# Kernel tuning notes

Hardware: AMD Instinct MI355X
Metric: run time of the kernel (lower is better)

## Reference

```python
import jax, jax.numpy as jnp
import numpy as np
from jax import lax

B, L, DDYN, DSTAT, H = 512, 64, 16, 8, 512
N_BANK, C_CAND, K_TOP, N_PROTO = 50000, 1024, 16, 8
T_TARG, Q_QUANT = 2, 3
TEMP = 0.2


def _l2norm(x, eps=1e-12):
    # matches torch.nn.functional.normalize: x / max(||x||, eps)
    n = jnp.sqrt(jnp.sum(x * x, axis=-1, keepdims=True))
    return x / jnp.maximum(n, eps)


def setup_inputs() -> dict:
    key = jax.random.key(0)
    ks = jax.random.split(key, 24)
    s = 0.02
    inp = {
        'sequence_values': jax.random.normal(ks[0], (B, L, DDYN), jnp.float32),
        'sequence_masks': jnp.ones((B, L), jnp.float32),
        'static_values': jax.random.normal(ks[1], (B, DSTAT), jnp.float32),
        'bank_keys': jax.random.normal(ks[2], (N_BANK, H), jnp.float32),
        'bank_values': jax.random.normal(ks[3], (N_BANK, H), jnp.float32),
        'candidate_indices': jax.random.randint(ks[4], (B, C_CAND), 0, N_BANK, jnp.int64),
        # encoder params (SequenceEncoder stand-in: masked-mean + linear + relu)
        'W_seq': jax.random.normal(ks[5], (DDYN, H), jnp.float32) * s,
        'W_stat': jax.random.normal(ks[6], (DSTAT, H), jnp.float32) * s,
        'b_enc': jnp.zeros((H,), jnp.float32),
        # retrieval / prototype / fusion params
        'W_q': jax.random.normal(ks[7], (H, H), jnp.float32) * s,
        'b_q': jnp.zeros((H,), jnp.float32),
        'prototype_tokens': jax.random.normal(ks[8], (N_PROTO, H), jnp.float32) * 0.02,
        'W_tr': jax.random.normal(ks[9], (2 * H, H), jnp.float32) * s,
        'b_tr': jnp.zeros((H,), jnp.float32),
        'W_gate': jax.random.normal(ks[10], (3 * H, H), jnp.float32) * s,
        'b_gate': jnp.zeros((H,), jnp.float32),
        'W_out': jax.random.normal(ks[11], (H, H), jnp.float32) * s,
        'b_out': jnp.zeros((H,), jnp.float32),
        # per-target heads stacked: [T, H, Q] and [T, H]
        'W_quant': jax.random.normal(ks[12], (T_TARG, H, Q_QUANT), jnp.float32) * s,
        'b_quant': jnp.zeros((T_TARG, Q_QUANT), jnp.float32),
        'W_ev': jax.random.normal(ks[13], (T_TARG, H), jnp.float32) * s,
        'b_ev': jnp.zeros((T_TARG,), jnp.float32),
    }
    return inp


def reference(sequence_values, sequence_masks, static_values, bank_keys, bank_values,
              candidate_indices, W_seq, W_stat, b_enc, W_q, b_q, prototype_tokens,
              W_tr, b_tr, W_gate, b_gate, W_out, b_out, W_quant, b_quant, W_ev, b_ev):
    # --- encoder (masked mean pool + linear + relu stand-in for SequenceEncoder) ---
    m = sequence_masks[..., None]                                   # [B,L,1]
    pooled = (sequence_values * m).sum(1) / jnp.maximum(m.sum(1), 1e-6)
    local_hidden = jax.nn.relu(pooled @ W_seq + static_values @ W_stat + b_enc)  # [B,H]

    # --- normalized query ---
    query = _l2norm(local_hidden @ W_q + b_q)                       # [B,H]

    # --- donor retrieval: gather + dot + topk + softmax + weighted sum ---
    cand_keys = bank_keys[candidate_indices]                        # [B,C,H]
    sim = jnp.einsum('bch,bh->bc', cand_keys, query)                # [B,C]
    top_scores, top_pos = lax.top_k(sim, K_TOP)                     # [B,K]
    weights = jax.nn.softmax(top_scores / max(TEMP, 1e-6), axis=-1)
    sel_idx = jnp.take_along_axis(candidate_indices, top_pos, axis=1)  # [B,K]
    donor_hidden = jnp.einsum('bk,bkh->bh', weights, bank_values[sel_idx])

    # --- prototype attention ---
    protos_n = _l2norm(prototype_tokens)                            # [P,H]
    pw = jax.nn.softmax(query @ protos_n.T, axis=-1)                # [B,P]
    proto_hidden = pw @ prototype_tokens                            # [B,H]

    # --- transfer / gate / fuse (dropout is identity at eval) ---
    transfer = jax.nn.relu(jnp.concatenate([donor_hidden, proto_hidden], -1) @ W_tr + b_tr)
    gate = jax.nn.sigmoid(
        jnp.concatenate([local_hidden, donor_hidden, proto_hidden], -1) @ W_gate + b_gate)
    fused = gate * local_hidden + (1.0 - gate) * transfer
    fused = jax.nn.relu(fused @ W_out + b_out)                      # [B,H]

    # --- heads: sorted quantiles [B,T,Q] and event logits [B,T] ---
    quant = jnp.sort(jnp.einsum('bh,thq->btq', fused, W_quant) + b_quant, axis=-1)
    logit = jnp.einsum('bh,th->bt', fused, W_ev) + b_ev
    return jnp.concatenate([quant.reshape(quant.shape[0], -1), logit], axis=-1)  # [B, T*Q+T]
```

## Files before the change

kernel.cpp:

```cpp
#include <hip/hip_runtime.h>
#include <hip/hip_bf16.h>

typedef __hip_bfloat16 bf16;

__device__ __forceinline__ float lo16(unsigned u){ return __uint_as_float(u << 16); }
__device__ __forceinline__ float hi16(unsigned u){ return __uint_as_float(u & 0xffff0000u); }

#define Bn 512
#define Hn 512
#define Cn 1024
#define Kn 16
#define NBANK 50000
#define NIDPAD 50176

__device__ __forceinline__ int clamp_id(int id){
    return (id < 0) ? 0 : ((id >= NBANK) ? (NBANK - 1) : id);
}

#define QRAW_OFF 0
#define F1_OFF   0
#define G_OFF    262144
#define DONOR_OFF (G_OFF + 262144)
#define PROTO_OFF (G_OFF + 524288)
#define SIM_OFF  1048576
#define F2_OFF   1048576
#define GATE_OFF 1572864
#define TR_OFF   1835008
#define WS_FLOATS 2097152

#define HIST_I   0
#define CURSOR_I NIDPAD
#define OFFS_I   (2*NIDPAD)
#define CHPREF_I (2*NIDPAD + NIDPAD)

__global__ __launch_bounds__(256) void k_enc(
    const float* __restrict__ seq, const float* __restrict__ mask, const float* __restrict__ stat,
    const float* __restrict__ W_seq, const float* __restrict__ W_stat, const float* __restrict__ b_enc,
    const int* __restrict__ cand32, float* __restrict__ ws)
{
    const int b = blockIdx.x, t = threadIdx.x;
    const int h0 = 2*t, h1 = 2*t + 1;

    {
        const int c64 = ((cand32[1] | cand32[3] | cand32[5] | cand32[7]) == 0) ? 1 : 0;
        int* hist = (int*)(ws + GATE_OFF) + HIST_I;
        #pragma unroll
        for (int u = 0; u < 4; u++) {
            int idx = b*Cn + u*256 + t;
            atomicAdd(&hist[clamp_id(cand32[(size_t)idx << c64])], 1);
        }
    }

    __shared__ float s_pool[16], s_stat[8];
    if (t < 16) {
        float acc = 0.f, ms = 0.f;
        for (int l = 0; l < 64; l++) {
            float m = mask[b*64 + l];
            ms  += m;
            acc += seq[(b*64 + l)*16 + t] * m;
        }
        s_pool[t] = acc / fmaxf(ms, 1e-6f);
    } else if (t < 24) {
        s_stat[t - 16] = stat[b*8 + (t - 16)];
    }
    __syncthreads();
    float a0 = b_enc[h0], a1 = b_enc[h1];
    #pragma unroll
    for (int j = 0; j < 16; j++) {
        float2 wv = *(const float2*)(W_seq + j*Hn + h0);
        a0 += s_pool[j]*wv.x; a1 += s_pool[j]*wv.y;
    }
    #pragma unroll
    for (int j = 0; j < 8; j++) {
        float2 wv = *(const float2*)(W_stat + j*Hn + h0);
        a0 += s_stat[j]*wv.x; a1 += s_stat[j]*wv.y;
    }
    float* g = ws + G_OFF + (size_t)b*Hn;
    g[h0] = fmaxf(a0, 0.f); g[h1] = fmaxf(a1, 0.f);
}

__global__ __launch_bounds__(256) void k_qgemm_sk(
    const float* __restrict__ W, const float* __restrict__ bias,
    const float* __restrict__ in, int in_stride, int in_off,
    float* __restrict__ outp)
{
    const int ct = blockIdx.x, rt = blockIdx.y, kz = blockIdx.z, t = threadIdx.x;
    __shared__ float lt[64][132];
    {
        int r = t >> 2, c0 = (t & 3)*32;
        const float* src = in + (size_t)(rt*64 + r)*in_stride + in_off + kz*128 + c0;
        #pragma unroll
        for (int i = 0; i < 8; i++)
            *(float4*)&lt[r][c0 + i*4] = *(const float4*)(src + i*4);
    }
    __syncthreads();
    const int col0 = ct*64 + (t & 15)*4, rbase = (t >> 4)*4;
    float acc[4][4];
    if (kz == 0) {
        float4 bv = *(const float4*)(bias + col0);
        #pragma unroll
        for (int i = 0; i < 4; i++) { acc[i][0]=bv.x; acc[i][1]=bv.y; acc[i][2]=bv.z; acc[i][3]=bv.w; }
    } else {
        #pragma unroll
        for (int i = 0; i < 4; i++) { acc[i][0]=0; acc[i][1]=0; acc[i][2]=0; acc[i][3]=0; }
    }
    const float* wp = W + (size_t)(kz*128)*Hn + col0;
    #pragma unroll 4
    for (int k = 0; k < 128; k++) {
        float4 wv = *(const float4*)(wp + (size_t)k*Hn);
        #pragma unroll
        for (int i = 0; i < 4; i++) {
            float a = lt[rbase + i][k];
            acc[i][0] += a*wv.x; acc[i][1] += a*wv.y; acc[i][2] += a*wv.z; acc[i][3] += a*wv.w;
        }
    }
    #pragma unroll
    for (int i = 0; i < 4; i++) {
        float* op = outp + (size_t)(rt*64 + rbase + i)*Hn + col0;
        atomicAdd(op+0, acc[i][0]); atomicAdd(op+1, acc[i][1]);
        atomicAdd(op+2, acc[i][2]); atomicAdd(op+3, acc[i][3]);
    }
}

__global__ __launch_bounds__(64) void k_qnorm(float* __restrict__ ws)
{
    const int b = blockIdx.x, lane = threadIdx.x;
    float* qr = ws + QRAW_OFF + (size_t)b*Hn + lane*8;
    float4 qa = *(const float4*)qr, qb = *(const float4*)(qr + 4);
    float ss = qa.x*qa.x + qa.y*qa.y + qa.z*qa.z + qa.w*qa.w
             + qb.x*qb.x + qb.y*qb.y + qb.z*qb.z + qb.w*qb.w;
    #pragma unroll
    for (int o = 32; o; o >>= 1) ss += __shfl_xor(ss, o);
    float inv = 1.f / fmaxf(sqrtf(ss), 1e-12f);
    qa.x *= inv; qa.y *= inv; qa.z *= inv; qa.w *= inv;
    qb.x *= inv; qb.y *= inv; qb.z *= inv; qb.w *= inv;
    *(float4*)qr = qa; *(float4*)(qr + 4) = qb;
}

__global__ __launch_bounds__(256) void k_scanA(
    const int* __restrict__ hist, int* __restrict__ offs, int* __restrict__ chsum)
{
    __shared__ int s[256];
    const int t = threadIdx.x, g = blockIdx.x*256 + t;
    const int v = hist[g];
    s[t] = v; __syncthreads();
    #pragma unroll
    for (int off = 1; off < 256; off <<= 1) {
        int x = (t >= off) ? s[t - off] : 0;
        __syncthreads();
        s[t] += x;
        __syncthreads();
    }
    offs[g] = s[t] - v;
    if (t == 255) chsum[blockIdx.x] = s[255];
}

__global__ __launch_bounds__(256) void k_scanB(int* __restrict__ chsum)
{
    __shared__ int s[256];
    const int t = threadIdx.x;
    const int v = (t < 196) ? chsum[t] : 0;
    s[t] = v; __syncthreads();
    #pragma unroll
    for (int off = 1; off < 256; off <<= 1) {
        int x = (t >= off) ? s[t - off] : 0;
        __syncthreads();
        s[t] += x;
        __syncthreads();
    }
    if (t < 196) chsum[t] = s[t] - v;
}

__global__ __launch_bounds__(256) void k_scatter(
    const int* __restrict__ cand32, int* __restrict__ cursor,
    const int* __restrict__ offs, const int* __restrict__ chpref,
    unsigned* __restrict__ refs)
{
    const int i = blockIdx.x*256 + threadIdx.x;
    const int c64 = ((cand32[1] | cand32[3] | cand32[5] | cand32[7]) == 0) ? 1 : 0;
    const int id = clamp_id(cand32[(size_t)i << c64]);
    const int pos = atomicAdd(&cursor[id], 1);
    refs[offs[id] + chpref[id >> 8] + pos] = (unsigned)i;
}

__global__ __launch_bounds__(256) void k_dotinv(
    const float* __restrict__ bank_keys, const unsigned* __restrict__ refs,
    const int* __restrict__ offs, const int* __restrict__ chpref,
    float* __restrict__ ws)
{
    const int id = blockIdx.x*4 + (threadIdx.x >> 6);
    const int lane = threadIdx.x & 63;
    const int start = offs[id]     + chpref[id >> 8];
    const int end   = offs[id + 1] + chpref[(id + 1) >> 8];
    if (start >= end) return;

    const float* kp = bank_keys + (size_t)id*Hn + lane*8;
    float4 ka = *(const float4*)kp, kb = *(const float4*)(kp + 4);
    const float* qbase = ws + QRAW_OFF;
    float* simw = ws + SIM_OFF;

    for (int r = start; r < end; r += 4) {
        const int nn = end - r;
        unsigned rv0 = refs[r];
        unsigned rv1 = refs[nn > 1 ? r + 1 : r];
        unsigned rv2 = refs[nn > 2 ? r + 2 : r];
        unsigned rv3 = refs[nn > 3 ? r + 3 : r];
        const float* q0 = qbase + (size_t)(rv0 >> 10)*Hn + lane*8;
        const float* q1 = qbase + (size_t)(rv1 >> 10)*Hn + lane*8;
        const float* q2 = qbase + (size_t)(rv2 >> 10)*Hn + lane*8;
        const float* q3 = qbase + (size_t)(rv3 >> 10)*Hn + lane*8;
        float4 a0 = *(const float4*)q0, b0 = *(const float4*)(q0 + 4);
        float4 a1 = *(const float4*)q1, b1 = *(const float4*)(q1 + 4);
        float4 a2 = *(const float4*)q2, b2 = *(const float4*)(q2 + 4);
        float4 a3 = *(const float4*)q3, b3 = *(const float4*)(q3 + 4);
        float s0 = ka.x*a0.x + ka.y*a0.y + ka.z*a0.z + ka.w*a0.w
                 + kb.x*b0.x + kb.y*b0.y + kb.z*b0.z + kb.w*b0.w;
        float s1 = ka.x*a1.x + ka.y*a1.y + ka.z*a1.z + ka.w*a1.w
                 + kb.x*b1.x + kb.y*b1.y + kb.z*b1.z + kb.w*b1.w;
        float s2 = ka.x*a2.x + ka.y*a2.y + ka.z*a2.z + ka.w*a2.w
                 + kb.x*b2.x + kb.y*b2.y + kb.z*b2.z + kb.w*b2.w;
        float s3 = ka.x*a3.x + ka.y*a3.y + ka.z*a3.z + ka.w*a3.w
                 + kb.x*b3.x + kb.y*b3.y + kb.z*b3.z + kb.w*b3.w;
        #pragma unroll
        for (int o = 32; o; o >>= 1) {
            s0 += __shfl_xor(s0, o); s1 += __shfl_xor(s1, o);
            s2 += __shfl_xor(s2, o); s3 += __shfl_xor(s3, o);
        }
        if (lane == 0) {
            simw[rv0] = s0;
            if (nn > 1) simw[rv1] = s1;
            if (nn > 2) simw[rv2] = s2;
            if (nn > 3) simw[rv3] = s3;
        }
    }
}

__global__ __launch_bounds__(256) void k_select(
    const float* __restrict__ bank_values, const int* __restrict__ cand32,
    const float* __restrict__ proto, float* __restrict__ ws)
{
    const int b = blockIdx.x, t = threadIdx.x;
    const int w = t >> 6, lane = t & 63;
    const int h0 = 2*t, h1 = 2*t + 1;
    const int c64 = ((cand32[1] | cand32[3] | cand32[5] | cand32[7]) == 0) ? 1 : 0;

    __shared__ __align__(16) float s_sim[Cn];
    __shared__ float s_bv[4]; __shared__ int s_bi[4];
    __shared__ float s_topv[Kn]; __shared__ int s_sel[Kn];
    __shared__ float s_w[Kn];
    __shared__ float s_score[8], s_pw[8];

    *(float4*)&s_sim[t*4] = *(const float4*)(ws + SIM_OFF + (size_t)b*Cn + t*4);

    const float* qr = ws + QRAW_OFF + (size_t)b*Hn + lane*8;
    float4 qa = *(const float4*)qr, qb = *(const float4*)(qr + 4);
    float qv[8] = {qa.x, qa.y, qa.z, qa.w, qb.x, qb.y, qb.z, qb.w};
    __syncthreads();

    for (int k = 0; k < Kn; k++) {
        float best = -1e30f; int bi = 0x7fffffff;
        for (int i = t; i < Cn; i += 256) {
            float v = s_sim[i];
            if (v > best || (v == best && i < bi)) { best = v; bi = i; }
        }
        #pragma unroll
        for (int o = 32; o; o >>= 1) {
            float ov = __shfl_xor(best, o); int oi = __shfl_xor(bi, o);
            if (ov > best || (ov == best && oi < bi)) { best = ov; bi = oi; }
        }
        if (lane == 0) { s_bv[w] = best; s_bi[w] = bi; }
        __syncthreads();
        if (t == 0) {
            float bv = s_bv[0]; int bbi = s_bi[0];
            for (int x = 1; x < 4; x++)
                if (s_bv[x] > bv || (s_bv[x] == bv && s_bi[x] < bbi)) { bv = s_bv[x]; bbi = s_bi[x]; }
            if (bbi < 0 || bbi >= Cn) bbi = 0;
            s_topv[k] = bv; s_sel[k] = bbi; s_sim[bbi] = -1e30f;
        }
        __syncthreads();
    }

    if (t == 0) {
        float m = s_topv[0];
        float e[Kn], ssum = 0.f;
        for (int k = 0; k < Kn; k++) { e[k] = __expf((s_topv[k] - m) * 5.0f); ssum += e[k]; }
        float inv = 1.f / ssum;
        for (int k = 0; k < Kn; k++) s_w[k] = e[k] * inv;
    }
    for (int p = w; p < 8; p += 4) {
        const float* pp = proto + (size_t)p*Hn + lane*8;
        float4 pa = *(const float4*)pp, pb = *(const float4*)(pp + 4);
        float f[8] = {pa.x, pa.y, pa.z, pa.w, pb.x, pb.y, pb.z, pb.w};
        float dq = 0.f, sq = 0.f;
        #pragma unroll
        for (int i = 0; i < 8; i++) { dq += f[i]*qv[i]; sq += f[i]*f[i]; }
        #pragma unroll
        for (int o = 32; o; o >>= 1) { dq += __shfl_xor(dq, o); sq += __shfl_xor(sq, o); }
        if (lane == 0) s_score[p] = dq / fmaxf(sqrtf(sq), 1e-12f);
    }
    __syncthreads();
    if (t == 0) {
        float m = s_score[0];
        for (int p = 1; p < 8; p++) m = fmaxf(m, s_score[p]);
        float e[8], ssum = 0.f;
        for (int p = 0; p < 8; p++) { e[p] = __expf(s_score[p] - m); ssum += e[p]; }
        float inv = 1.f / ssum;
        for (int p = 0; p < 8; p++) s_pw[p] = e[p] * inv;
    }
    __syncthreads();

    {
        float a0 = 0.f, a1 = 0.f;
        #pragma unroll
        for (int k = 0; k < Kn; k++) {
            int id = clamp_id(cand32[(size_t)(b*Cn + s_sel[k]) << c64]);
            float2 v = *(const float2*)(bank_values + (size_t)id*Hn + h0);
            a0 += s_w[k]*v.x; a1 += s_w[k]*v.y;
        }
        float* gd = ws + DONOR_OFF + (size_t)b*Hn;
        gd[h0] = a0; gd[h1] = a1;
    }
    {
        float a0 = 0.f, a1 = 0.f;
        #pragma unroll
        for (int p = 0; p < 8; p++) {
            float2 v = *(const float2*)(proto + (size_t)p*Hn + h0);
            a0 += s_pw[p]*v.x; a1 += s_pw[p]*v.y;
        }
        float* gp = ws + PROTO_OFF + (size_t)b*Hn;
        gp[h0] = a0; gp[h1] = a1;
    }
}

__global__ __launch_bounds__(256) void k_gatetr_sk(
    const float* __restrict__ W_tr, const float* __restrict__ b_tr,
    const float* __restrict__ W_gate, const float* __restrict__ b_gate,
    float* __restrict__ ws)
{
    const int ct = blockIdx.x, rt = blockIdx.y, z = blockIdx.z, t = threadIdx.x;
    const int isGate = (z < 6);
    const int slice = isGate ? z : (z - 6);
    const float* W  = isGate ? W_gate : W_tr;
    const int gcol = isGate ? slice*256 : 512 + slice*256;
    const float* srcbase = ws + G_OFF + (size_t)(gcol >> 9)*262144 + (gcol & 511);
    float* outp = ws + (isGate ? GATE_OFF : TR_OFF);

    __shared__ float lt[32][260];
    {
        int r = t >> 3, c0 = (t & 7)*32;
        const float* src = srcbase + (size_t)(rt*32 + r)*Hn + c0;
        #pragma unroll
        for (int i = 0; i < 8; i++)
            *(float4*)&lt[r][c0 + i*4] = *(const float4*)(src + i*4);
    }
    __syncthreads();
    const int col0 = ct*128 + (t & 31)*4, rbase = (t >> 5)*4;
    float acc[4][4];
    if (slice == 0) {
        const float* bias = isGate ? b_gate : b_tr;
        float4 bv = *(const float4*)(bias + col0);
        #pragma unroll
        for (int i = 0; i < 4; i++) { acc[i][0]=bv.x; acc[i][1]=bv.y; acc[i][2]=bv.z; acc[i][3]=bv.w; }
    } else {
        #pragma unroll
        for (int i = 0; i < 4; i++) { acc[i][0]=0; acc[i][1]=0; acc[i][2]=0; acc[i][3]=0; }
    }
    const float* wp = W + (size_t)(slice*256)*Hn + col0;
    #pragma unroll 4
    for (int k = 0; k < 256; k++) {
        float4 wv = *(const float4*)(wp + (size_t)k*Hn);
        #pragma unroll
        for (int i = 0; i < 4; i++) {
            float a = lt[rbase + i][k];
            acc[i][0] += a*wv.x; acc[i][1] += a*wv.y; acc[i][2] += a*wv.z; acc[i][3] += a*wv.w;
        }
    }
    #pragma unroll
    for (int i = 0; i < 4; i++) {
        float* op = outp + (size_t)(rt*32 + rbase + i)*Hn + col0;
        atomicAdd(op+0, acc[i][0]); atomicAdd(op+1, acc[i][1]);
        atomicAdd(op+2, acc[i][2]); atomicAdd(op+3, acc[i][3]);
    }
}

__global__ __launch_bounds__(256) void k_f1ew(float* __restrict__ ws)
{
    const int i4 = blockIdx.x*256 + threadIdx.x;
    const int row = i4 >> 7, c = (i4 & 127)*4;
    float4 lc = *(const float4*)(ws + G_OFF + (size_t)row*Hn + c);
    float4 ga = *(const float4*)(ws + GATE_OFF + (size_t)row*Hn + c);
    float4 tr = *(const float4*)(ws + TR_OFF + (size_t)row*Hn + c);
    float4 r;
    float s;
    s = 1.f/(1.f + __expf(-ga.x)); r.x = s*lc.x + (1.f-s)*fmaxf(tr.x, 0.f);
    s = 1.f/(1.f + __expf(-ga.y)); r.y = s*lc.y + (1.f-s)*fmaxf(tr.y, 0.f);
    s = 1.f/(1.f + __expf(-ga.z)); r.z = s*lc.z + (1.f-s)*fmaxf(tr.z, 0.f);
    s = 1.f/(1.f + __expf(-ga.w)); r.w = s*lc.w + (1.f-s)*fmaxf(tr.w, 0.f);
    *(float4*)(ws + F1_OFF + (size_t)row*Hn + c) = r;
}

__global__ __launch_bounds__(64) void k_heads(
    const float* __restrict__ W_quant, const float* __restrict__ b_quant,
    const float* __restrict__ W_ev, const float* __restrict__ b_ev,
    const float* __restrict__ ws_ro, float* __restrict__ out)
{
    const int b = blockIdx.x, lane = threadIdx.x;
    const float* fr = ws_ro + F2_OFF + (size_t)b*Hn + lane*8;
    float4 fa = *(const float4*)fr, fb = *(const float4*)(fr + 4);
    float fv[8] = {fmaxf(fa.x,0.f), fmaxf(fa.y,0.f), fmaxf(fa.z,0.f), fmaxf(fa.w,0.f),
                   fmaxf(fb.x,0.f), fmaxf(fb.y,0.f), fmaxf(fb.z,0.f), fmaxf(fb.w,0.f)};
    float acc[8];
    #pragma unroll
    for (int o = 0; o < 8; o++) acc[o] = 0.f;
    #pragma unroll
    for (int i = 0; i < 8; i++) {
        int h = lane*8 + i;
        float fh = fv[i];
        acc[0] += fh*W_quant[(0*Hn + h)*3 + 0];
        acc[1] += fh*W_quant[(0*Hn + h)*3 + 1];
        acc[2] += fh*W_quant[(0*Hn + h)*3 + 2];
        acc[3] += fh*W_quant[(1*Hn + h)*3 + 0];
        acc[4] += fh*W_quant[(1*Hn + h)*3 + 1];
        acc[5] += fh*W_quant[(1*Hn + h)*3 + 2];
        acc[6] += fh*W_ev[0*Hn + h];
        acc[7] += fh*W_ev[1*Hn + h];
    }
    #pragma unroll
    for (int o = 0; o < 8; o++) {
        #pragma unroll
        for (int s = 32; s; s >>= 1) acc[o] += __shfl_xor(acc[o], s);
    }
    if (lane == 0) {
        float q[6];
        for (int o = 0; o < 6; o++) q[o] = acc[o] + b_quant[o];
        #pragma unroll
        for (int tt = 0; tt < 2; tt++) {
            float a = q[tt*3], bb = q[tt*3+1], c = q[tt*3+2];
            float mn = fminf(a, fminf(bb, c)), mx = fmaxf(a, fmaxf(bb, c));
            float md = a + bb + c - mn - mx;
            q[tt*3] = mn; q[tt*3+1] = md; q[tt*3+2] = mx;
        }
        for (int o = 0; o < 6; o++) out[b*8 + o] = q[o];
        out[b*8 + 6] = acc[6] + b_ev[0];
        out[b*8 + 7] = acc[7] + b_ev[1];
    }
}

__device__ __forceinline__ float lds_f(const void* p, int i, int f32){
    return f32 ? ((const float*)p)[i] : __bfloat162float(((const bf16*)p)[i]);
}
__device__ __forceinline__ float2 ldpair(const void* p, int elt, int f32){
    if (f32) return ((const float2*)p)[elt >> 1];
    unsigned u = ((const unsigned*)p)[elt >> 1];
    return make_float2(lo16(u), hi16(u));
}
__device__ __forceinline__ void ld8(const void* p, int elt, int f32, float* v){
    if (f32){
        const float4* q = (const float4*)((const float*)p + elt);
        float4 a = q[0], b = q[1];
        v[0]=a.x; v[1]=a.y; v[2]=a.z; v[3]=a.w; v[4]=b.x; v[5]=b.y; v[6]=b.z; v[7]=b.w;
    } else {
        uint4 u = *(const uint4*)((const bf16*)p + elt);
        v[0]=lo16(u.x); v[1]=hi16(u.x); v[2]=lo16(u.y); v[3]=hi16(u.y);
        v[4]=lo16(u.z); v[5]=hi16(u.z); v[6]=lo16(u.w); v[7]=hi16(u.w);
    }
}
__device__ __forceinline__ void st_out(void* o, int i, int f32, float v){
    if (f32) ((float*)o)[i] = v; else ((bf16*)o)[i] = __float2bfloat16(v);
}

__global__ __launch_bounds__(256) void k_fused(
    const void* __restrict__ seq, const void* __restrict__ mask, const void* __restrict__ stat,
    const void* __restrict__ bank_keys, const void* __restrict__ bank_values,
    const int* __restrict__ cand32,
    const void* __restrict__ W_seq, const void* __restrict__ W_stat, const void* __restrict__ b_enc,
    const void* __restrict__ W_q, const void* __restrict__ b_q,
    const void* __restrict__ proto,
    const void* __restrict__ W_tr, const void* __restrict__ b_tr,
    const void* __restrict__ W_gate, const void* __restrict__ b_gate,
    const void* __restrict__ W_out, const void* __restrict__ b_out,
    const void* __restrict__ W_quant, const void* __restrict__ b_quant,
    const void* __restrict__ W_ev, const void* __restrict__ b_ev,
    void* __restrict__ out)
{
    const int b = blockIdx.x, t = threadIdx.x;
    const int w = t >> 6, lane = t & 63;
    const int h0 = 2*t, h1 = 2*t + 1;
    const int f32 = (((const unsigned short*)mask)[0] == 0) ? 1 : 0;
    const int c64 = ((cand32[1] | cand32[3] | cand32[5] | cand32[7]) == 0) ? 1 : 0;

    __shared__ __align__(16) float s_pool[16];
    __shared__ __align__(16) float s_stat[8];
    __shared__ __align__(16) float g[1536];
    __shared__ __align__(16) float s_q[Hn];
    __shared__ __align__(16) float s_sim[Cn];
    __shared__ __align__(16) float f1[Hn];
    __shared__ __align__(16) float f2[Hn];
    __shared__ float s_part[4], s_ss;
    __shared__ float s_bv[4]; __shared__ int s_bi[4];
    __shared__ float s_topv[Kn]; __shared__ int s_sel[Kn];
    __shared__ float s_w[Kn];
    __shared__ float s_score[8], s_pw[8];
    __shared__ float s_head[8][4];

    if (t < 16) {
        float acc = 0.f, ms = 0.f;
        for (int l = 0; l < 64; l++) {
            float m = lds_f(mask, b*64 + l, f32);
            ms  += m;
            acc += lds_f(seq, (b*64 + l)*16 + t, f32) * m;
        }
        s_pool[t] = acc / fmaxf(ms, 1e-6f);
    } else if (t < 24) {
        s_stat[t - 16] = lds_f(stat, b*8 + (t - 16), f32);
    }
    __syncthreads();
    {
        float a0 = lds_f(b_enc, h0, f32), a1 = lds_f(b_enc, h1, f32);
        #pragma unroll
        for (int j = 0; j < 16; j++) {
            float2 wv = ldpair(W_seq, j*Hn + h0, f32);
            a0 += s_pool[j]*wv.x; a1 += s_pool[j]*wv.y;
        }
        #pragma unroll
        for (int j = 0; j < 8; j++) {
// ... 131 lines not shown
        gt0 += gj*wv.x; gt1 += gj*wv.y;
    }
    gt0 = 1.f/(1.f + __expf(-gt0)); gt1 = 1.f/(1.f + __expf(-gt1));
    f1[h0] = gt0*g[h0] + (1.f - gt0)*tr0;
    f1[h1] = gt1*g[h1] + (1.f - gt1)*tr1;
    __syncthreads();
    {
        float o0 = lds_f(b_out, h0, f32), o1 = lds_f(b_out, h1, f32);
        #pragma unroll 4
        for (int j = 0; j < Hn; j++) {
            float fj = f1[j];
            float2 wv = ldpair(W_out, j*Hn + h0, f32);
            o0 += fj*wv.x; o1 += fj*wv.y;
        }
        o0 = fmaxf(o0, 0.f); o1 = fmaxf(o1, 0.f);
        f2[h0] = o0; f2[h1] = o1;
    }
    __syncthreads();
    {
        float acc[8];
        #pragma unroll
        for (int o = 0; o < 8; o++) acc[o] = 0.f;
        for (int h = t; h < Hn; h += 256) {
            float fh = f2[h];
            acc[0] += fh*lds_f(W_quant, (0*Hn + h)*3 + 0, f32);
            acc[1] += fh*lds_f(W_quant, (0*Hn + h)*3 + 1, f32);
            acc[2] += fh*lds_f(W_quant, (0*Hn + h)*3 + 2, f32);
            acc[3] += fh*lds_f(W_quant, (1*Hn + h)*3 + 0, f32);
            acc[4] += fh*lds_f(W_quant, (1*Hn + h)*3 + 1, f32);
            acc[5] += fh*lds_f(W_quant, (1*Hn + h)*3 + 2, f32);
            acc[6] += fh*lds_f(W_ev, 0*Hn + h, f32);
            acc[7] += fh*lds_f(W_ev, 1*Hn + h, f32);
        }
        #pragma unroll
        for (int o = 0; o < 8; o++) {
            float v = acc[o];
            #pragma unroll
            for (int s = 32; s; s >>= 1) v += __shfl_xor(v, s);
            if (lane == 0) s_head[o][w] = v;
        }
        __syncthreads();
        if (t == 0) {
            float q[6];
            for (int o = 0; o < 6; o++)
                q[o] = s_head[o][0] + s_head[o][1] + s_head[o][2] + s_head[o][3] + lds_f(b_quant, o, f32);
            #pragma unroll
            for (int tt = 0; tt < 2; tt++) {
                float a = q[tt*3], bb = q[tt*3+1], c = q[tt*3+2];
                float mn = fminf(a, fminf(bb, c)), mx = fmaxf(a, fmaxf(bb, c));
                float md = a + bb + c - mn - mx;
                q[tt*3] = mn; q[tt*3+1] = md; q[tt*3+2] = mx;
            }
            for (int o = 0; o < 6; o++) st_out(out, b*8 + o, f32, q[o]);
            float l0 = s_head[6][0] + s_head[6][1] + s_head[6][2] + s_head[6][3] + lds_f(b_ev, 0, f32);
            float l1 = s_head[7][0] + s_head[7][1] + s_head[7][2] + s_head[7][3] + lds_f(b_ev, 1, f32);
            st_out(out, b*8 + 6, f32, l0);
            st_out(out, b*8 + 7, f32, l1);
        }
    }
}

extern "C" void kernel_launch(void* const* d_in, const int* in_sizes, int n_in,
                              void* d_out, int out_size, void* d_ws, size_t ws_size,
                              hipStream_t stream) {
    static const int expect[22] = {
        512*64*16, 512*64, 512*8, 50000*512, 50000*512, 512*1024,
        16*512, 8*512, 512, 512*512, 512, 8*512,
        1024*512, 512, 1536*512, 512, 512*512, 512,
        2*512*3, 2*3, 2*512, 2
    };
    if (n_in != 22 || out_size != 512*8) return;
    for (int i = 0; i < 22; i++) if (in_sizes[i] != expect[i]) return;

    if (ws_size < (size_t)WS_FLOATS * 4) {
        k_fused<<<Bn, 256, 0, stream>>>(
            d_in[0], d_in[1], d_in[2], d_in[3], d_in[4], (const int*)d_in[5],
            d_in[6], d_in[7], d_in[8], d_in[9], d_in[10], d_in[11],
            d_in[12], d_in[13], d_in[14], d_in[15], d_in[16], d_in[17],
            d_in[18], d_in[19], d_in[20], d_in[21], d_out);
        return;
    }

    float* ws = (float*)d_ws;
    int* iws = (int*)(ws + GATE_OFF);
    int* hist   = iws + HIST_I;
    int* cursor = iws + CURSOR_I;
    int* offs   = iws + OFFS_I;
    int* chpref = iws + CHPREF_I;
    unsigned* refs = (unsigned*)(ws + DONOR_OFF);

    hipMemsetAsync(ws + QRAW_OFF, 0, (size_t)512*512*4, stream);
    hipMemsetAsync(hist, 0, (size_t)2*NIDPAD*4, stream);
    hipMemsetAsync(ws + TR_OFF, 0, (size_t)512*512*4, stream);

    k_enc<<<Bn, 256, 0, stream>>>((const float*)d_in[0], (const float*)d_in[1],
                                  (const float*)d_in[2], (const float*)d_in[6],
                                  (const float*)d_in[7], (const float*)d_in[8],
                                  (const int*)d_in[5], ws);
    k_scanA<<<NIDPAD/256, 256, 0, stream>>>(hist, offs, chpref);
    k_scanB<<<1, 256, 0, stream>>>(chpref);
    k_scatter<<<(Bn*Cn)/256, 256, 0, stream>>>((const int*)d_in[5], cursor, offs, chpref, refs);
    k_qgemm_sk<<<dim3(8, 8, 4), 256, 0, stream>>>(
        (const float*)d_in[9], (const float*)d_in[10], ws + G_OFF, 512, 0, ws + QRAW_OFF);
    k_qnorm<<<Bn, 64, 0, stream>>>(ws);
    k_dotinv<<<NBANK/4, 256, 0, stream>>>((const float*)d_in[3], refs, offs, chpref, ws);
    k_select<<<Bn, 256, 0, stream>>>((const float*)d_in[4], (const int*)d_in[5],
                                     (const float*)d_in[11], ws);
    hipMemsetAsync(ws + GATE_OFF, 0, (size_t)512*512*4, stream);
    hipMemsetAsync(ws + F2_OFF, 0, (size_t)512*512*4, stream);
    k_gatetr_sk<<<dim3(4, 16, 10), 256, 0, stream>>>(
        (const float*)d_in[12], (const float*)d_in[13],
        (const float*)d_in[14], (const float*)d_in[15], ws);
    k_f1ew<<<256, 256, 0, stream>>>(ws);
    k_qgemm_sk<<<dim3(8, 8, 4), 256, 0, stream>>>(
        (const float*)d_in[16], (const float*)d_in[17], ws + F1_OFF, 512, 0, ws + F2_OFF);
    k_heads<<<Bn, 64, 0, stream>>>((const float*)d_in[18], (const float*)d_in[19],
                                   (const float*)d_in[20], (const float*)d_in[21],
                                   ws, (float*)d_out);
}
```

Measured before the change: 546.8 us.

## Replace split-K atomics with partial buffers, single-pass scan, pipelined dot kernel

The split-K GEMMs now write plain float4 partial results into separate workspace slabs, and the consumers (qnorm, f1ew, heads) sum those partials. This removes the float atomics and most of the large memsets. The two-level scan is merged into one kernel that takes block bases from a global atomic counter. The dot-inverse kernel is software-pipelined with double-buffered loads, shuffles refs from a register, and reduces four dot products at once. The trade-off is extra reads of the partial buffers and a workspace layout that has to stay consistent across every stage.

```diff
diff --git a/kernel.cpp b/kernel.cpp
--- a/kernel.cpp
+++ b/kernel.cpp
@@ -17,21 +17,21 @@
     return (id < 0) ? 0 : ((id >= NBANK) ? (NBANK - 1) : id);
 }
 
-#define QRAW_OFF 0
-#define F1_OFF   0
-#define G_OFF    262144
-#define DONOR_OFF (G_OFF + 262144)
-#define PROTO_OFF (G_OFF + 524288)
+#define A_OFF    0
+#define B_OFF    262144
+#define C_OFF    524288
+#define D_OFF    786432
 #define SIM_OFF  1048576
-#define F2_OFF   1048576
-#define GATE_OFF 1572864
-#define TR_OFF   1835008
+#define ELO_OFF  1048576
+#define EHI_OFF  1310720
+#define F_OFF    1572864
+#define G_OFF2   1835008
 #define WS_FLOATS 2097152
 
 #define HIST_I   0
 #define CURSOR_I NIDPAD
-#define OFFS_I   (2*NIDPAD)
-#define CHPREF_I (2*NIDPAD + NIDPAD)
+#define GTOT_I   (2*NIDPAD)
+#define OFFS_I   (2*NIDPAD + 256)
 
 __global__ __launch_bounds__(256) void k_enc(
     const float* __restrict__ seq, const float* __restrict__ mask, const float* __restrict__ stat,
@@ -43,7 +43,7 @@
 
     {
         const int c64 = ((cand32[1] | cand32[3] | cand32[5] | cand32[7]) == 0) ? 1 : 0;
-        int* hist = (int*)(ws + GATE_OFF) + HIST_I;
+        int* hist = (int*)(ws + F_OFF) + HIST_I;
         #pragma unroll
         for (int u = 0; u < 4; u++) {
             int idx = b*Cn + u*256 + t;
@@ -75,20 +75,51 @@
         float2 wv = *(const float2*)(W_stat + j*Hn + h0);
         a0 += s_stat[j]*wv.x; a1 += s_stat[j]*wv.y;
     }
-    float* g = ws + G_OFF + (size_t)b*Hn;
+    float* g = ws + B_OFF + (size_t)b*Hn;
     g[h0] = fmaxf(a0, 0.f); g[h1] = fmaxf(a1, 0.f);
 }
 
-__global__ __launch_bounds__(256) void k_qgemm_sk(
+__global__ __launch_bounds__(256) void k_scan(
+    const int* __restrict__ hist, int* __restrict__ offs, int* __restrict__ gtot)
+{
+    __shared__ int s[256]; __shared__ int sbase;
+    const int t = threadIdx.x, g = blockIdx.x*256 + t;
+    const int v = hist[g];
+    s[t] = v; __syncthreads();
+    #pragma unroll
+    for (int off = 1; off < 256; off <<= 1) {
+        int x = (t >= off) ? s[t - off] : 0;
+        __syncthreads();
+        s[t] += x;
+        __syncthreads();
+    }
+    if (t == 255) sbase = atomicAdd(gtot, s[255]);
+    __syncthreads();
+    offs[g] = sbase + s[t] - v;
+}
+
+__global__ __launch_bounds__(256) void k_scatter(
+    const int* __restrict__ cand32, int* __restrict__ cursor,
+    const int* __restrict__ offs, unsigned* __restrict__ refs)
+{
+    const int i = blockIdx.x*256 + threadIdx.x;
+    const int c64 = ((cand32[1] | cand32[3] | cand32[5] | cand32[7]) == 0) ? 1 : 0;
+    const int id = clamp_id(cand32[(size_t)i << c64]);
+    const int pos = atomicAdd(&cursor[id], 1);
+    refs[offs[id] + pos] = (unsigned)i;
+}
+
+__global__ __launch_bounds__(256) void k_qgemm_p(
     const float* __restrict__ W, const float* __restrict__ bias,
-    const float* __restrict__ in, int in_stride, int in_off,
-    float* __restrict__ outp)
+    const float* __restrict__ in,
+    float* __restrict__ P0, float* __restrict__ P1,
+    float* __restrict__ P2, float* __restrict__ P3)
 {
     const int ct = blockIdx.x, rt = blockIdx.y, kz = blockIdx.z, t = threadIdx.x;
     __shared__ float lt[64][132];
     {
         int r = t >> 2, c0 = (t & 3)*32;
-        const float* src = in + (size_t)(rt*64 + r)*in_stride + in_off + kz*128 + c0;
+        const float* src = in + (size_t)(rt*64 + r)*Hn + kz*128 + c0;
         #pragma unroll
         for (int i = 0; i < 8; i++)
             *(float4*)&lt[r][c0 + i*4] = *(const float4*)(src + i*4);
@@ -114,124 +145,119 @@
             acc[i][0] += a*wv.x; acc[i][1] += a*wv.y; acc[i][2] += a*wv.z; acc[i][3] += a*wv.w;
         }
     }
+    float* outp = (kz == 0) ? P0 : (kz == 1) ? P1 : (kz == 2) ? P2 : P3;
     #pragma unroll
     for (int i = 0; i < 4; i++) {
         float* op = outp + (size_t)(rt*64 + rbase + i)*Hn + col0;
-        atomicAdd(op+0, acc[i][0]); atomicAdd(op+1, acc[i][1]);
-        atomicAdd(op+2, acc[i][2]); atomicAdd(op+3, acc[i][3]);
-    }
-}
-
-__global__ __launch_bounds__(64) void k_qnorm(float* __restrict__ ws)
-{
-    const int b = blockIdx.x, lane = threadIdx.x;
-    float* qr = ws + QRAW_OFF + (size_t)b*Hn + lane*8;
-    float4 qa = *(const float4*)qr, qb = *(const float4*)(qr + 4);
+        *(float4*)op = make_float4(acc[i][0], acc[i][1], acc[i][2], acc[i][3]);
+    }
+}
+
+__global__ __launch_bounds__(256) void k_qnorm(float* __restrict__ ws)
+{
+    const int b = blockIdx.x*4 + (threadIdx.x >> 6), lane = threadIdx.x & 63;
+    const size_t o = (size_t)b*Hn + lane*8;
+    const float* p0 = ws + A_OFF   + o;
+    const float* p1 = ws + ELO_OFF + o;
+    const float* p2 = ws + EHI_OFF + o;
+    const float* p3 = ws + G_OFF2  + o;
+    float4 qa, qb;
+    {
+        float4 a0 = *(const float4*)p0, a1 = *(const float4*)p1,
+               a2 = *(const float4*)p2, a3 = *(const float4*)p3;
+        qa = make_float4(((a0.x+a1.x)+a2.x)+a3.x, ((a0.y+a1.y)+a2.y)+a3.y,
+                         ((a0.z+a1.z)+a2.z)+a3.z, ((a0.w+a1.w)+a2.w)+a3.w);
+        float4 b0 = *(const float4*)(p0+4), b1 = *(const float4*)(p1+4),
+               b2 = *(const float4*)(p2+4), b3 = *(const float4*)(p3+4);
+        qb = make_float4(((b0.x+b1.x)+b2.x)+b3.x, ((b0.y+b1.y)+b2.y)+b3.y,
+                         ((b0.z+b1.z)+b2.z)+b3.z, ((b0.w+b1.w)+b2.w)+b3.w);
+    }
     float ss = qa.x*qa.x + qa.y*qa.y + qa.z*qa.z + qa.w*qa.w
              + qb.x*qb.x + qb.y*qb.y + qb.z*qb.z + qb.w*qb.w;
     #pragma unroll
-    for (int o = 32; o; o >>= 1) ss += __shfl_xor(ss, o);
+    for (int o2 = 32; o2; o2 >>= 1) ss += __shfl_xor(ss, o2);
     float inv = 1.f / fmaxf(sqrtf(ss), 1e-12f);
     qa.x *= inv; qa.y *= inv; qa.z *= inv; qa.w *= inv;
     qb.x *= inv; qb.y *= inv; qb.z *= inv; qb.w *= inv;
+    float* qr = ws + A_OFF + o;
     *(float4*)qr = qa; *(float4*)(qr + 4) = qb;
 }
 
-__global__ __launch_bounds__(256) void k_scanA(
-    const int* __restrict__ hist, int* __restrict__ offs, int* __restrict__ chsum)
-{
-    __shared__ int s[256];
-    const int t = threadIdx.x, g = blockIdx.x*256 + t;
-    const int v = hist[g];
-    s[t] = v; __syncthreads();
-    #pragma unroll
-    for (int off = 1; off < 256; off <<= 1) {
-        int x = (t >= off) ? s[t - off] : 0;
-        __syncthreads();
-        s[t] += x;
-        __syncthreads();
-    }
-    offs[g] = s[t] - v;
-    if (t == 255) chsum[blockIdx.x] = s[255];
-}
-
-__global__ __launch_bounds__(256) void k_scanB(int* __restrict__ chsum)
-{
-    __shared__ int s[256];
-    const int t = threadIdx.x;
-    const int v = (t < 196) ? chsum[t] : 0;
-    s[t] = v; __syncthreads();
-    #pragma unroll
-    for (int off = 1; off < 256; off <<= 1) {
-        int x = (t >= off) ? s[t - off] : 0;
-        __syncthreads();
-        s[t] += x;
-        __syncthreads();
-    }
-    if (t < 196) chsum[t] = s[t] - v;
-}
-
-__global__ __launch_bounds__(256) void k_scatter(
-    const int* __restrict__ cand32, int* __restrict__ cursor,
-    const int* __restrict__ offs, const int* __restrict__ chpref,
-    unsigned* __restrict__ refs)
-{
-    const int i = blockIdx.x*256 + threadIdx.x;
-    const int c64 = ((cand32[1] | cand32[3] | cand32[5] | cand32[7]) == 0) ? 1 : 0;
-    const int id = clamp_id(cand32[(size_t)i << c64]);
-    const int pos = atomicAdd(&cursor[id], 1);
-    refs[offs[id] + chpref[id >> 8] + pos] = (unsigned)i;
-}
-
-__global__ __launch_bounds__(256) void k_dotinv(
+#define DI_LOAD(R0,R1,R2,R3,A0,Bq0,A1,Bq1,A2,Bq2,A3,Bq3,BASE) do {                       \
+    int m_ = n - 1;                                                                      \
+    int j0_=(BASE), j1_=(BASE)+1, j2_=(BASE)+2, j3_=(BASE)+3;                            \
+    j0_ = j0_>m_?m_:j0_; j1_ = j1_>m_?m_:j1_; j2_ = j2_>m_?m_:j2_; j3_ = j3_>m_?m_:j3_;  \
+    R0 = (j0_<64)?(unsigned)__shfl((int)refv,j0_):refs[start+j0_];                       \
+    R1 = (j1_<64)?(unsigned)__shfl((int)refv,j1_):refs[start+j1_];                       \
+    R2 = (j2_<64)?(unsigned)__shfl((int)refv,j2_):refs[start+j2_];                       \
+    R3 = (j3_<64)?(unsigned)__shfl((int)refv,j3_):refs[start+j3_];                       \
+    const float* q0_ = qbase + (size_t)(R0>>10)*Hn + lane*8;                             \
+    const float* q1_ = qbase + (size_t)(R1>>10)*Hn + lane*8;                             \
+    const float* q2_ = qbase + (size_t)(R2>>10)*Hn + lane*8;                             \
+    const float* q3_ = qbase + (size_t)(R3>>10)*Hn + lane*8;                             \
+    A0 = *(const float4*)q0_; Bq0 = *(const float4*)(q0_+4);                             \
+    A1 = *(const float4*)q1_; Bq1 = *(const float4*)(q1_+4);                             \
+    A2 = *(const float4*)q2_; Bq2 = *(const float4*)(q2_+4);                             \
+    A3 = *(const float4*)q3_; Bq3 = *(const float4*)(q3_+4);                             \
+} while(0)
+
+#define DI_COMP(R0,R1,R2,R3,A0,Bq0,A1,Bq1,A2,Bq2,A3,Bq3,BASE) do {                       \
+    float s0_ = ka.x*A0.x + ka.y*A0.y + ka.z*A0.z + ka.w*A0.w                            \
+              + kb.x*Bq0.x + kb.y*Bq0.y + kb.z*Bq0.z + kb.w*Bq0.w;                       \
+    float s1_ = ka.x*A1.x + ka.y*A1.y + ka.z*A1.z + ka.w*A1.w                            \
+              + kb.x*Bq1.x + kb.y*Bq1.y + kb.z*Bq1.z + kb.w*Bq1.w;                       \
+    float s2_ = ka.x*A2.x + ka.y*A2.y + ka.z*A2.z + ka.w*A2.w                            \
+              + kb.x*Bq2.x + kb.y*Bq2.y + kb.z*Bq2.z + kb.w*Bq2.w;                       \
+    float s3_ = ka.x*A3.x + ka.y*A3.y + ka.z*A3.z + ka.w*A3.w                            \
+              + kb.x*Bq3.x + kb.y*Bq3.y + kb.z*Bq3.z + kb.w*Bq3.w;                       \
+    s0_ += __shfl_xor(s0_,32); s1_ += __shfl_xor(s1_,32);                                \
+    s2_ += __shfl_xor(s2_,32); s3_ += __shfl_xor(s3_,32);                                \
+    s0_ += __shfl_xor(s0_,16); s1_ += __shfl_xor(s1_,16);                                \
+    s2_ += __shfl_xor(s2_,16); s3_ += __shfl_xor(s3_,16);                                \
+    s0_ += __shfl_xor(s0_, 8); s1_ += __shfl_xor(s1_, 8);                                \
+    s2_ += __shfl_xor(s2_, 8); s3_ += __shfl_xor(s3_, 8);                                \
+    int d_ = (lane >> 3) & 3;                                                            \
+    float t_ = d_==0 ? s0_ : d_==1 ? s1_ : d_==2 ? s2_ : s3_;                            \
+    t_ += __shfl_xor(t_, 4); t_ += __shfl_xor(t_, 2); t_ += __shfl_xor(t_, 1);           \
+    if ((lane & 7) == 0 && lane < 32) {                                                  \
+        int dd_ = lane >> 3;                                                             \
+        if ((BASE) + dd_ < n) {                                                          \
+            unsigned rs_ = dd_==0 ? R0 : dd_==1 ? R1 : dd_==2 ? R2 : R3;                 \
+            simw[rs_] = t_;                                                              \
+        }                                                                                \
+    }                                                                                    \
+} while(0)
+
+__global__ __launch_bounds__(256, 4) void k_dotinv(
     const float* __restrict__ bank_keys, const unsigned* __restrict__ refs,
-    const int* __restrict__ offs, const int* __restrict__ chpref,
+    const int* __restrict__ offs, const int* __restrict__ cnt,
     float* __restrict__ ws)
 {
     const int id = blockIdx.x*4 + (threadIdx.x >> 6);
     const int lane = threadIdx.x & 63;
-    const int start = offs[id]     + chpref[id >> 8];
-    const int end   = offs[id + 1] + chpref[(id + 1) >> 8];
-    if (start >= end) return;
+    const int n = cnt[id];
+    if (n <= 0) return;
+    const int start = offs[id];
 
     const float* kp = bank_keys + (size_t)id*Hn + lane*8;
     float4 ka = *(const float4*)kp, kb = *(const float4*)(kp + 4);
-    const float* qbase = ws + QRAW_OFF;
+    const unsigned refv = refs[start + (lane < n ? lane : n - 1)];
+    const float* qbase = ws + A_OFF;
     float* simw = ws + SIM_OFF;
 
-    for (int r = start; r < end; r += 4) {
-        const int nn = end - r;
-        unsigned rv0 = refs[r];
-        unsigned rv1 = refs[nn > 1 ? r + 1 : r];
-        unsigned rv2 = refs[nn > 2 ? r + 2 : r];
-        unsigned rv3 = refs[nn > 3 ? r + 3 : r];
-        const float* q0 = qbase + (size_t)(rv0 >> 10)*Hn + lane*8;
-        const float* q1 = qbase + (size_t)(rv1 >> 10)*Hn + lane*8;
-        const float* q2 = qbase + (size_t)(rv2 >> 10)*Hn + lane*8;
-        const float* q3 = qbase + (size_t)(rv3 >> 10)*Hn + lane*8;
-        float4 a0 = *(const float4*)q0, b0 = *(const float4*)(q0 + 4);
-        float4 a1 = *(const float4*)q1, b1 = *(const float4*)(q1 + 4);
-        float4 a2 = *(const float4*)q2, b2 = *(const float4*)(q2 + 4);
-        float4 a3 = *(const float4*)q3, b3 = *(const float4*)(q3 + 4);
-        float s0 = ka.x*a0.x + ka.y*a0.y + ka.z*a0.z + ka.w*a0.w
-                 + kb.x*b0.x + kb.y*b0.y + kb.z*b0.z + kb.w*b0.w;
-        float s1 = ka.x*a1.x + ka.y*a1.y + ka.z*a1.z + ka.w*a1.w
-                 + kb.x*b1.x + kb.y*b1.y + kb.z*b1.z + kb.w*b1.w;
-        float s2 = ka.x*a2.x + ka.y*a2.y + ka.z*a2.z + ka.w*a2.w
-                 + kb.x*b2.x + kb.y*b2.y + kb.z*b2.z + kb.w*b2.w;
-        float s3 = ka.x*a3.x + ka.y*a3.y + ka.z*a3.z + ka.w*a3.w
-                 + kb.x*b3.x + kb.y*b3.y + kb.z*b3.z + kb.w*b3.w;
-        #pragma unroll
-        for (int o = 32; o; o >>= 1) {
-            s0 += __shfl_xor(s0, o); s1 += __shfl_xor(s1, o);
-            s2 += __shfl_xor(s2, o); s3 += __shfl_xor(s3, o);
-        }
-        if (lane == 0) {
-            simw[rv0] = s0;
-            if (nn > 1) simw[rv1] = s1;
-            if (nn > 2) simw[rv2] = s2;
-            if (nn > 3) simw[rv3] = s3;
-        }
+    unsigned Ar0,Ar1,Ar2,Ar3, Br0=0,Br1=0,Br2=0,Br3=0;
+    float4 Aa0,Ab0,Aa1,Ab1,Aa2,Ab2,Aa3,Ab3;
+    float4 Ba0,Bb0,Ba1,Bb1,Ba2,Bb2,Ba3,Bb3;
+    Ba0=Bb0=Ba1=Bb1=Ba2=Bb2=Ba3=Bb3=make_float4(0.f,0.f,0.f,0.f);
+
+    DI_LOAD(Ar0,Ar1,Ar2,Ar3, Aa0,Ab0,Aa1,Ab1,Aa2,Ab2,Aa3,Ab3, 0);
+    for (int base = 0; ; ) {
+        if (base + 4 < n) DI_LOAD(Br0,Br1,Br2,Br3, Ba0,Bb0,Ba1,Bb1,Ba2,Bb2,Ba3,Bb3, base + 4);
+        DI_COMP(Ar0,Ar1,Ar2,Ar3, Aa0,Ab0,Aa1,Ab1,Aa2,Ab2,Aa3,Ab3, base);
+        if (base + 8 < n) DI_LOAD(Ar0,Ar1,Ar2,Ar3, Aa0,Ab0,Aa1,Ab1,Aa2,Ab2,Aa3,Ab3, base + 8);
+        DI_COMP(Br0,Br1,Br2,Br3, Ba0,Bb0,Ba1,Bb1,Ba2,Bb2,Ba3,Bb3, base + 4);
+        base += 8;
+        if (base >= n) break;
     }
 }
 
@@ -252,7 +278,7 @@
 
     *(float4*)&s_sim[t*4] = *(const float4*)(ws + SIM_OFF + (size_t)b*Cn + t*4);
 
-    const float* qr = ws + QRAW_OFF + (size_t)b*Hn + lane*8;
+    const float* qr = ws + A_OFF + (size_t)b*Hn + lane*8;
     float4 qa = *(const float4*)qr, qb = *(const float4*)(qr + 4);
     float qv[8] = {qa.x, qa.y, qa.z, qa.w, qb.x, qb.y, qb.z, qb.w};
     __syncthreads();
@@ -317,7 +343,7 @@
             float2 v = *(const float2*)(bank_values + (size_t)id*Hn + h0);
             a0 += s_w[k]*v.x; a1 += s_w[k]*v.y;
         }
-        float* gd = ws + DONOR_OFF + (size_t)b*Hn;
+        float* gd = ws + C_OFF + (size_t)b*Hn;
         gd[h0] = a0; gd[h1] = a1;
     }
     {
@@ -327,36 +353,29 @@
             float2 v = *(const float2*)(proto + (size_t)p*Hn + h0);
             a0 += s_pw[p]*v.x; a1 += s_pw[p]*v.y;
         }
-        float* gp = ws + PROTO_OFF + (size_t)b*Hn;
+        float* gp = ws + D_OFF + (size_t)b*Hn;
         gp[h0] = a0; gp[h1] = a1;
     }
 }
 
-__global__ __launch_bounds__(256) void k_gatetr_sk(
+__global__ __launch_bounds__(256) void k_gatetr_p(
     const float* __restrict__ W_tr, const float* __restrict__ b_tr,
     const float* __restrict__ W_gate, const float* __restrict__ b_gate,
     float* __restrict__ ws)
 {
     const int ct = blockIdx.x, rt = blockIdx.y, z = blockIdx.z, t = threadIdx.x;
-    const int isGate = (z < 6);
-    const int slice = isGate ? z : (z - 6);
-    const float* W  = isGate ? W_gate : W_tr;
-    const int gcol = isGate ? slice*256 : 512 + slice*256;
-    const float* srcbase = ws + G_OFF + (size_t)(gcol >> 9)*262144 + (gcol & 511);
-    float* outp = ws + (isGate ? GATE_OFF : TR_OFF);
+    const int isGate = (z < 3);
+    const int sl = isGate ? z : (z - 3);
+    const float* W = isGate ? (W_gate + (size_t)(z*512)*Hn) : (W_tr + (size_t)(sl*512)*Hn);
+    const float* slab = ws + B_OFF + (size_t)(isGate ? z : (sl + 1))*262144;
+    float* outp = isGate
+        ? ((z == 0) ? ws + A_OFF : (z == 1) ? ws + ELO_OFF : ws + EHI_OFF)
+        : ((sl == 0) ? ws + F_OFF : ws + G_OFF2);
 
     __shared__ float lt[32][260];
-    {
-        int r = t >> 3, c0 = (t & 7)*32;
-        const float* src = srcbase + (size_t)(rt*32 + r)*Hn + c0;
-        #pragma unroll
-        for (int i = 0; i < 8; i++)
-            *(float4*)&lt[r][c0 + i*4] = *(const float4*)(src + i*4);
-    }
-    __syncthreads();
     const int col0 = ct*128 + (t & 31)*4, rbase = (t >> 5)*4;
     float acc[4][4];
-    if (slice == 0) {
+    if (z == 0 || z == 3) {
         const float* bias = isGate ? b_gate : b_tr;
         float4 bv = *(const float4*)(bias + col0);
         #pragma unroll
@@ -365,38 +384,56 @@
         #pragma unroll
         for (int i = 0; i < 4; i++) { acc[i][0]=0; acc[i][1]=0; acc[i][2]=0; acc[i][3]=0; }
     }
-    const float* wp = W + (size_t)(slice*256)*Hn + col0;
-    #pragma unroll 4
-    for (int k = 0; k < 256; k++) {
-        float4 wv = *(const float4*)(wp + (size_t)k*Hn);
-        #pragma unroll
-        for (int i = 0; i < 4; i++) {
-            float a = lt[rbase + i][k];
-            acc[i][0] += a*wv.x; acc[i][1] += a*wv.y; acc[i][2] += a*wv.z; acc[i][3] += a*wv.w;
+
+    #pragma unroll
+    for (int h = 0; h < 2; h++) {
+        if (h) __syncthreads();
+        {
+            int r = t >> 3, c0 = (t & 7)*32;
+            const float* src = slab + (size_t)(rt*32 + r)*Hn + h*256 + c0;
+            #pragma unroll
+            for (int i = 0; i < 8; i++)
+                *(float4*)&lt[r][c0 + i*4] = *(const float4*)(src + i*4);
+        }
+        __syncthreads();
+        const float* wp = W + (size_t)(h*256)*Hn + col0;
+        #pragma unroll 4
+        for (int k = 0; k < 256; k++) {
+            float4 wv = *(const float4*)(wp + (size_t)k*Hn);
+            #pragma unroll
+            for (int i = 0; i < 4; i++) {
+                float a = lt[rbase + i][k];
+                acc[i][0] += a*wv.x; acc[i][1] += a*wv.y; acc[i][2] += a*wv.z; acc[i][3] += a*wv.w;
+            }
         }
     }
     #pragma unroll
     for (int i = 0; i < 4; i++) {
         float* op = outp + (size_t)(rt*32 + rbase + i)*Hn + col0;
-        atomicAdd(op+0, acc[i][0]); atomicAdd(op+1, acc[i][1]);
-        atomicAdd(op+2, acc[i][2]); atomicAdd(op+3, acc[i][3]);
+        *(float4*)op = make_float4(acc[i][0], acc[i][1], acc[i][2], acc[i][3]);
     }
 }
 
 __global__ __launch_bounds__(256) void k_f1ew(float* __restrict__ ws)
 {
     const int i4 = blockIdx.x*256 + threadIdx.x;
-    const int row = i4 >> 7, c = (i4 & 127)*4;
-    float4 lc = *(const float4*)(ws + G_OFF + (size_t)row*Hn + c);
-    float4 ga = *(const float4*)(ws + GATE_OFF + (size_t)row*Hn + c);
-    float4 tr = *(const float4*)(ws + TR_OFF + (size_t)row*Hn + c);
+    const size_t off = (size_t)(i4 >> 7)*Hn + (i4 & 127)*4;
+    float4 lc = *(const float4*)(ws + B_OFF + off);
+    float4 g0 = *(const float4*)(ws + A_OFF + off);
+    float4 g1 = *(const float4*)(ws + ELO_OFF + off);
+    float4 g2 = *(const float4*)(ws + EHI_OFF + off);
+    float4 t0 = *(const float4*)(ws + F_OFF + off);
+    float4 t1 = *(const float4*)(ws + G_OFF2 + off);
+    float4 ga = make_float4((g0.x+g1.x)+g2.x, (g0.y+g1.y)+g2.y,
+                            (g0.z+g1.z)+g2.z, (g0.w+g1.w)+g2.w);
+    float4 tr = make_float4(t0.x+t1.x, t0.y+t1.y, t0.z+t1.z, t0.w+t1.w);
     float4 r;
     float s;
     s = 1.f/(1.f + __expf(-ga.x)); r.x = s*lc.x + (1.f-s)*fmaxf(tr.x, 0.f);
     s = 1.f/(1.f + __expf(-ga.y)); r.y = s*lc.y + (1.f-s)*fmaxf(tr.y, 0.f);
     s = 1.f/(1.f + __expf(-ga.z)); r.z = s*lc.z + (1.f-s)*fmaxf(tr.z, 0.f);
     s = 1.f/(1.f + __expf(-ga.w)); r.w = s*lc.w + (1.f-s)*fmaxf(tr.w, 0.f);
-    *(float4*)(ws + F1_OFF + (size_t)row*Hn + c) = r;
+    *(float4*)(ws + A_OFF + off) = r;
 }
 
 __global__ __launch_bounds__(64) void k_heads(
@@ -405,13 +442,23 @@
     const float* __restrict__ ws_ro, float* __restrict__ out)
 {
     const int b = blockIdx.x, lane = threadIdx.x;
-    const float* fr = ws_ro + F2_OFF + (size_t)b*Hn + lane*8;
-    float4 fa = *(const float4*)fr, fb = *(const float4*)(fr + 4);
-    float fv[8] = {fmaxf(fa.x,0.f), fmaxf(fa.y,0.f), fmaxf(fa.z,0.f), fmaxf(fa.w,0.f),
-                   fmaxf(fb.x,0.f), fmaxf(fb.y,0.f), fmaxf(fb.z,0.f), fmaxf(fb.w,0.f)};
+    const size_t o = (size_t)b*Hn + lane*8;
+    const float* p0 = ws_ro + ELO_OFF + o;
+    const float* p1 = ws_ro + EHI_OFF + o;
+    const float* p2 = ws_ro + F_OFF + o;
+    const float* p3 = ws_ro + G_OFF2 + o;
+    float4 a0 = *(const float4*)p0, a1 = *(const float4*)p1,
+           a2 = *(const float4*)p2, a3 = *(const float4*)p3;
+    float4 b0 = *(const float4*)(p0+4), b1 = *(const float4*)(p1+4),
+           b2 = *(const float4*)(p2+4), b3 = *(const float4*)(p3+4);
+    float fv[8] = {
+        fmaxf(((a0.x+a1.x)+a2.x)+a3.x, 0.f), fmaxf(((a0.y+a1.y)+a2.y)+a3.y, 0.f),
+        fmaxf(((a0.z+a1.z)+a2.z)+a3.z, 0.f), fmaxf(((a0.w+a1.w)+a2.w)+a3.w, 0.f),
+        fmaxf(((b0.x+b1.x)+b2.x)+b3.x, 0.f), fmaxf(((b0.y+b1.y)+b2.y)+b3.y, 0.f),
+        fmaxf(((b0.z+b1.z)+b2.z)+b3.z, 0.f), fmaxf(((b0.w+b1.w)+b2.w)+b3.w, 0.f)};
     float acc[8];
     #pragma unroll
-    for (int o = 0; o < 8; o++) acc[o] = 0.f;
+    for (int q = 0; q < 8; q++) acc[q] = 0.f;
     #pragma unroll
     for (int i = 0; i < 8; i++) {
         int h = lane*8 + i;
@@ -426,21 +473,21 @@
         acc[7] += fh*W_ev[1*Hn + h];
     }
     #pragma unroll
-    for (int o = 0; o < 8; o++) {
-        #pragma unroll
-        for (int s = 32; s; s >>= 1) acc[o] += __shfl_xor(acc[o], s);
+    for (int q = 0; q < 8; q++) {
+        #pragma unroll
+        for (int s = 32; s; s >>= 1) acc[q] += __shfl_xor(acc[q], s);
     }
     if (lane == 0) {
-        float q[6];
-        for (int o = 0; o < 6; o++) q[o] = acc[o] + b_quant[o];
+        float qv[6];
+        for (int q = 0; q < 6; q++) qv[q] = acc[q] + b_quant[q];
         #pragma unroll
         for (int tt = 0; tt < 2; tt++) {
-            float a = q[tt*3], bb = q[tt*3+1], c = q[tt*3+2];
+            float a = qv[tt*3], bb = qv[tt*3+1], c = qv[tt*3+2];
             float mn = fminf(a, fminf(bb, c)), mx = fmaxf(a, fmaxf(bb, c));
             float md = a + bb + c - mn - mx;
-            q[tt*3] = mn; q[tt*3+1] = md; q[tt*3+2] = mx;
-        }
-        for (int o = 0; o < 6; o++) out[b*8 + o] = q[o];
+            qv[tt*3] = mn; qv[tt*3+1] = md; qv[tt*3+2] = mx;
+        }
+        for (int q = 0; q < 6; q++) out[b*8 + q] = qv[q];
         out[b*8 + 6] = acc[6] + b_ev[0];
         out[b*8 + 7] = acc[7] + b_ev[1];
     }
@@ -738,38 +785,35 @@
     }
 
     float* ws = (float*)d_ws;
-    int* iws = (int*)(ws + GATE_OFF);
+    int* iws = (int*)(ws + F_OFF);
     int* hist   = iws + HIST_I;
     int* cursor = iws + CURSOR_I;
+    int* gtot   = iws + GTOT_I;
     int* offs   = iws + OFFS_I;
-    int* chpref = iws + CHPREF_I;
-    unsigned* refs = (unsigned*)(ws + DONOR_OFF);
-
-    hipMemsetAsync(ws + QRAW_OFF, 0, (size_t)512*512*4, stream);
-    hipMemsetAsync(hist, 0, (size_t)2*NIDPAD*4, stream);
-    hipMemsetAsync(ws + TR_OFF, 0, (size_t)512*512*4, stream);
+    unsigned* refs = (unsigned*)(ws + C_OFF);
+
+    hipMemsetAsync(iws, 0, (size_t)(2*NIDPAD + 256)*4, stream);
 
     k_enc<<<Bn, 256, 0, stream>>>((const float*)d_in[0], (const float*)d_in[1],
                                   (const float*)d_in[2], (const float*)d_in[6],
                                   (const float*)d_in[7], (const float*)d_in[8],
                                   (const int*)d_in[5], ws);
-    k_scanA<<<NIDPAD/256, 256, 0, stream>>>(hist, offs, chpref);
-    k_scanB<<<1, 256, 0, stream>>>(chpref);
-    k_scatter<<<(Bn*Cn)/256, 256, 0, stream>>>((const int*)d_in[5], cursor, offs, chpref, refs);
-    k_qgemm_sk<<<dim3(8, 8, 4), 256, 0, stream>>>(
-        (const float*)d_in[9], (const float*)d_in[10], ws + G_OFF, 512, 0, ws + QRAW_OFF);
-    k_qnorm<<<Bn, 64, 0, stream>>>(ws);
-    k_dotinv<<<NBANK/4, 256, 0, stream>>>((const float*)d_in[3], refs, offs, chpref, ws);
+    k_scan<<<NIDPAD/256, 256, 0, stream>>>(hist, offs, gtot);
+    k_scatter<<<(Bn*Cn)/256, 256, 0, stream>>>((const int*)d_in[5], cursor, offs, refs);
+    k_qgemm_p<<<dim3(8, 8, 4), 256, 0, stream>>>(
+        (const float*)d_in[9], (const float*)d_in[10], ws + B_OFF,
+        ws + A_OFF, ws + ELO_OFF, ws + EHI_OFF, ws + G_OFF2);
+    k_qnorm<<<Bn/4, 256, 0, stream>>>(ws);
+    k_dotinv<<<NBANK/4, 256, 0, stream>>>((const float*)d_in[3], refs, offs, hist, ws);
     k_select<<<Bn, 256, 0, stream>>>((const float*)d_in[4], (const int*)d_in[5],
                                      (const float*)d_in[11], ws);
-    hipMemsetAsync(ws + GATE_OFF, 0, (size_t)512*512*4, stream);
-    hipMemsetAsync(ws + F2_OFF, 0, (size_t)512*512*4, stream);
-    k_gatetr_sk<<<dim3(4, 16, 10), 256, 0, stream>>>(
+    k_gatetr_p<<<dim3(4, 16, 5), 256, 0, stream>>>(
         (const float*)d_in[12], (const float*)d_in[13],
         (const float*)d_in[14], (const float*)d_in[15], ws);
     k_f1ew<<<256, 256, 0, stream>>>(ws);
-    k_qgemm_sk<<<dim3(8, 8, 4), 256, 0, stream>>>(
-        (const float*)d_in[16], (const float*)d_in[17], ws + F1_OFF, 512, 0, ws + F2_OFF);
+    k_qgemm_p<<<dim3(8, 8, 4), 256, 0, stream>>>(
+        (const float*)d_in[16], (const float*)d_in[17], ws + A_OFF,
+        ws + ELO_OFF, ws + EHI_OFF, ws + F_OFF, ws + G_OFF2);
     k_heads<<<Bn, 64, 0, stream>>>((const float*)d_in[18], (const float*)d_in[19],
                                    (const float*)d_in[20], (const float*)d_in[21],
                                    ws, (float*)d_out);
```

Measured after the change: 508.1 us. 7.1% less time.
